# Kernel tuning notes

Measured on AMD Instinct MI355X. Metric: run time of the kernel, lower is better.

## Reference

```python
import jax, jax.numpy as jnp
import numpy as np

EMBED = 768
HEADS = 12
HEAD_DIM = EMBED // HEADS
RATES = (1, 2, 4)
SEGS = (2048, 4096, 8192)


def setup_inputs() -> dict:
    key = jax.random.key(0)
    k1, k2, k3 = jax.random.split(key, 3)
    b, n = 2, 8192
    x = jax.random.normal(k1, (b, n, EMBED), dtype=jnp.float32)
    Wqkv = jax.random.normal(k2, (3 * EMBED, EMBED), dtype=jnp.float32) * 0.02
    Wout = jax.random.normal(k3, (EMBED, EMBED), dtype=jnp.float32) * 0.02
    return {"x": x, "Wqkv": Wqkv, "Wout": Wout}


def _dilated_attention(qkv):
    # qkv: [b, n, 3, h, d]
    b, n, _, h, d = qkv.shape
    scale = 1.0 / jnp.sqrt(jnp.asarray(d, qkv.dtype))
    out = jnp.zeros((b, n, h, d), dtype=qkv.dtype)
    for r, s in zip(RATES, SEGS):
        sr = s // r
        nseg = n // s
        # strided gather: [b, nseg, sr, 3, h, d]
        g = qkv.reshape(b, nseg, s, 3, h, d)[:, :, ::r]
        # fold stride offset into batch; attention runs over the segment axis
        g = g.transpose(0, 2, 1, 3, 4, 5).reshape(b * sr, nseg, 3, h, d)
        q, k, v = g[:, :, 0], g[:, :, 1], g[:, :, 2]
        scores = jnp.einsum('bnhd,bmhd->bhnm', q, k) * scale
        attn = jax.nn.softmax(scores, axis=-1)
        o = jnp.einsum('bhnm,bmhd->bnhd', attn, v)
        # scatter-add back into strided positions
        o = o.reshape(b, sr, nseg, h, d).transpose(0, 2, 1, 3, 4)
        out = out.reshape(b, nseg, s, h, d).at[:, :, ::r].add(o).reshape(b, n, h, d)
    # normalize over full sequence dim (as in original module)
    out = out / out.sum(axis=1, keepdims=True)
    return out


def reference(x, Wqkv, Wout):
    b, n, e = x.shape
    qkv = (x @ Wqkv.T).reshape(b, n, 3, HEADS, HEAD_DIM)
    o = _dilated_attention(qkv)  # [b, n, h, d]
    return o.reshape(b, n, e) @ Wout.T
```

## Files before the change

kernel.cpp:

```cpp
#include <hip/hip_runtime.h>

typedef unsigned short u16;
typedef __attribute__((ext_vector_type(8))) short bf16x8;
typedef __attribute__((ext_vector_type(4))) float f32x4;

__device__ __forceinline__ u16 f2bf_rne(float f) {
  unsigned u = __float_as_uint(f);
  u += 0x7fffu + ((u >> 16) & 1u);
  return (u16)(u >> 16);
}
__device__ __forceinline__ float bf2f(u16 h) {
  return __uint_as_float(((unsigned)h) << 16);
}
__device__ __forceinline__ void split1(float v, u16& h, u16& l) {
  u16 hh = f2bf_rne(v);
  h = hh;
  l = f2bf_rne(v - bf2f(hh));
}

__device__ __forceinline__ void gl16(const void* g, void* l) {
  __builtin_amdgcn_global_load_lds(
      (const __attribute__((address_space(1))) unsigned int*)g,
      (__attribute__((address_space(3))) unsigned int*)l,
      16, 0, 0);
}

__global__ void split_convert_all(const float4* __restrict__ x,
                                  ushort4* __restrict__ xhi, ushort4* __restrict__ xlo,
                                  const float4* __restrict__ wq,
                                  ushort4* __restrict__ wqh, ushort4* __restrict__ wql,
                                  const float4* __restrict__ wo,
                                  ushort4* __restrict__ woh, ushort4* __restrict__ wol) {
  int i = blockIdx.x * 256 + threadIdx.x;
  const float4* src;
  ushort4 *dh, *dl;
  int idx;
  if (i < 3145728) { src = x; dh = xhi; dl = xlo; idx = i; }
  else if (i < 3588096) { src = wq; dh = wqh; dl = wql; idx = i - 3145728; }
  else if (i < 3735552) { src = wo; dh = woh; dl = wol; idx = i - 3588096; }
  else return;
  float4 v = src[idx];
  ushort4 h, l;
  split1(v.x, h.x, l.x); split1(v.y, h.y, l.y);
  split1(v.z, h.z, l.z); split1(v.w, h.w, l.w);
  dh[idx] = h; dl[idx] = l;
}

__global__ __launch_bounds__(256, 2) void gemm_split_bt(
    const u16* __restrict__ Ahi, const u16* __restrict__ Alo,
    const u16* __restrict__ Bhi, const u16* __restrict__ Blo,
    float* __restrict__ C, int M, int N, int K) {
  __shared__ __align__(16) u16 sAh[128 * 64], sAl[128 * 64], sBh[128 * 64], sBl[128 * 64];
  const int tid = threadIdx.x;
  const int wave = tid >> 6;
  const int lane = tid & 63;
  const int tm0 = blockIdx.x * 128;
  const int tn0 = blockIdx.y * 128;
  const int wm = (wave & 1) * 64;
  const int wn = (wave >> 1) * 64;

  const int srow = wave * 32 + (lane >> 3);
  const int c = lane & 7;
  const int scol = (c ^ ((lane >> 3) & 7)) * 8;
  const u16* gAh = Ahi + (size_t)(tm0 + srow) * K + scol;
  const u16* gAl = Alo + (size_t)(tm0 + srow) * K + scol;
  const u16* gBh = Bhi + (size_t)(tn0 + srow) * K + scol;
  const u16* gBl = Blo + (size_t)(tn0 + srow) * K + scol;
  u16* lAh = &sAh[wave * 32 * 64];
  u16* lAl = &sAl[wave * 32 * 64];
  u16* lBh = &sBh[wave * 32 * 64];
  u16* lBl = &sBl[wave * 32 * 64];
  const size_t rstep8 = (size_t)8 * K;

  f32x4 acc[4][4] = {};
  const int fr = lane & 15;
  const int quad = lane >> 4;

  for (int kt = 0; kt < K; kt += 64) {
#pragma unroll
    for (int r = 0; r < 4; ++r) {
      gl16(gAh + kt + r * rstep8, lAh + r * 512);
      gl16(gAl + kt + r * rstep8, lAl + r * 512);
      gl16(gBh + kt + r * rstep8, lBh + r * 512);
      gl16(gBl + kt + r * rstep8, lBl + r * 512);
    }
    __syncthreads();
    for (int subk = 0; subk < 2; ++subk) {
      const int k0 = ((subk * 4 + quad) ^ (fr & 7)) * 8;
      bf16x8 ah[4], al[4], bh[4], bl[4];
#pragma unroll
      for (int i = 0; i < 4; ++i) {
        ah[i] = *(const bf16x8*)&sAh[(wm + i * 16 + fr) * 64 + k0];
        al[i] = *(const bf16x8*)&sAl[(wm + i * 16 + fr) * 64 + k0];
        bh[i] = *(const bf16x8*)&sBh[(wn + i * 16 + fr) * 64 + k0];
        bl[i] = *(const bf16x8*)&sBl[(wn + i * 16 + fr) * 64 + k0];
      }
#pragma unroll
      for (int i = 0; i < 4; ++i)
#pragma unroll
        for (int j = 0; j < 4; ++j) {
          acc[i][j] = __builtin_amdgcn_mfma_f32_16x16x32_bf16(ah[i], bh[j], acc[i][j], 0, 0, 0);
          acc[i][j] = __builtin_amdgcn_mfma_f32_16x16x32_bf16(ah[i], bl[j], acc[i][j], 0, 0, 0);
          acc[i][j] = __builtin_amdgcn_mfma_f32_16x16x32_bf16(al[i], bh[j], acc[i][j], 0, 0, 0);
        }
    }
    __syncthreads();
  }

  const int col = lane & 15;
  const int rowq = (lane >> 4) * 4;
#pragma unroll
  for (int i = 0; i < 4; ++i)
#pragma unroll
    for (int j = 0; j < 4; ++j) {
      size_t base = (size_t)(tm0 + wm + i * 16 + rowq) * N + (tn0 + wn + j * 16 + col);
#pragma unroll
      for (int r = 0; r < 4; ++r) C[base + (size_t)r * N] = acc[i][j][r];
    }
}

__global__ __launch_bounds__(256) void attn_dilated(const float* __restrict__ qkv,
                                                    float* __restrict__ out) {
  __shared__ float rows[4][2304];
  __shared__ float sc[12][16];
  __shared__ float Aw[12][16];
  const int t = threadIdx.x;
  const int i0 = blockIdx.x;
  const int b = blockIdx.y;
  const size_t rowbase = (size_t)b * 8192 + i0;

  for (int idx = t; idx < 4 * 576; idx += 256) {
    int j = idx / 576, c4 = idx - j * 576;
    ((float4*)rows[j])[c4] = ((const float4*)(qkv + (rowbase + 2048 * j) * 2304))[c4];
  }
  __syncthreads();

  if (t < 192) {
    int h = t >> 4, j = (t >> 2) & 3, jp = t & 3;
    const float* q = &rows[j][h * 64];
    const float* k = &rows[jp][768 + h * 64];
    float s = 0.f;
#pragma unroll
    for (int d = 0; d < 64; ++d) s = fmaf(q[d], k[d], s);
    sc[h][(j << 2) | jp] = s * 0.125f;
  }
  __syncthreads();

  if (t < 48) {
    int h = t >> 2, j = t & 3;
    float s0 = sc[h][j * 4 + 0], s1 = sc[h][j * 4 + 1];
    float s2 = sc[h][j * 4 + 2], s3 = sc[h][j * 4 + 3];
    float m = fmaxf(fmaxf(s0, s1), fmaxf(s2, s3));
    float e0 = expf(s0 - m), e1 = expf(s1 - m), e2 = expf(s2 - m), e3 = expf(s3 - m);
    float inv = 1.f / (e0 + e1 + e2 + e3);
    float a[4] = {e0 * inv, e1 * inv, e2 * inv, e3 * inv};
    if ((i0 & 1) == 0) {
      int p = j ^ 2;
      float ss = sc[h][j * 4 + j], sx = sc[h][j * 4 + p];
      float mm = fmaxf(ss, sx);
      float es = expf(ss - mm), ex = expf(sx - mm);
      float iv = 1.f / (es + ex);
      a[j] += es * iv;
      a[p] += ex * iv;
    }
    if ((i0 & 3) == 0) a[j] += 1.f;
    Aw[h][j * 4 + 0] = a[0]; Aw[h][j * 4 + 1] = a[1];
    Aw[h][j * 4 + 2] = a[2]; Aw[h][j * 4 + 3] = a[3];
  }
  __syncthreads();

#pragma unroll
  for (int j = 0; j < 4; ++j) {
#pragma unroll
    for (int rep = 0; rep < 3; ++rep) {
      int cc = rep * 256 + t;
      int h = cc >> 6;
      float v = 0.f;
#pragma unroll
      for (int jp = 0; jp < 4; ++jp) v = fmaf(Aw[h][(j << 2) | jp], rows[jp][1536 + cc], v);
      out[(rowbase + 2048 * j) * 768 + cc] = v;
    }
  }
}

__global__ void colsum(const float* __restrict__ o, float* __restrict__ S) {
  int t = threadIdx.x;
  int rg = blockIdx.x;
  int cg = blockIdx.y;
  int b = blockIdx.z;
  int c = cg * 256 + t;
  const float* p = o + ((size_t)b * 8192 + (size_t)rg * 128) * 768 + c;
  float s = 0.f;
  for (int r = 0; r < 128; ++r) s += p[(size_t)r * 768];
  atomicAdd(&S[b * 768 + c], s);
}

__global__ void invk(float* S, int n) {
  int i = blockIdx.x * 256 + threadIdx.x;
  if (i < n) S[i] = 1.0f / S[i];
}

__global__ void norm_split4(const float4* __restrict__ in, const float* __restrict__ Sinv,
                            ushort4* __restrict__ hi, ushort4* __restrict__ lo, int n4) {
  int i = blockIdx.x * 256 + threadIdx.x;
  if (i >= n4) return;
  int e = i * 4;
  int c = e % 768;
  int b = e / (8192 * 768);
  const float* s = Sinv + b * 768 + c;
  float4 v = in[i];
  v.x *= s[0]; v.y *= s[1]; v.z *= s[2]; v.w *= s[3];
  ushort4 h, l;
  split1(v.x, h.x, l.x); split1(v.y, h.y, l.y);
  split1(v.z, h.z, l.z); split1(v.w, h.w, l.w);
  hi[i] = h; lo[i] = l;
}

extern "C" void kernel_launch(void* const* d_in, const int* in_sizes, int n_in,
                              void* d_out, int out_size, void* d_ws, size_t ws_size,
                              hipStream_t stream) {
  (void)in_sizes; (void)n_in; (void)out_size; (void)ws_size;
  const float* x = (const float*)d_in[0];
  const float* Wqkv = (const float*)d_in[1];
  const float* Wout = (const float*)d_in[2];
  float* out = (float*)d_out;

  char* w = (char*)d_ws;
  float* qkv = (float*)(w);
  u16* no_hi = (u16*)(w);
  u16* no_lo = (u16*)(w + 25165824);
  size_t off = 150994944;
  u16* xhi = (u16*)(w + off); off += 25165824;
  u16* xlo = (u16*)(w + off); off += 25165824;
  u16* wqh = (u16*)(w + off); off += 3538944;
  u16* wql = (u16*)(w + off); off += 3538944;
  u16* woh = (u16*)(w + off); off += 1179648;
  u16* wol = (u16*)(w + off); off += 1179648;
  float* S = (float*)(w + off); off += 6144;

  split_convert_all<<<dim3(14592), 256, 0, stream>>>(
      (const float4*)x, (ushort4*)xhi, (ushort4*)xlo,
      (const float4*)Wqkv, (ushort4*)wqh, (ushort4*)wql,
      (const float4*)Wout, (ushort4*)woh, (ushort4*)wol);

  gemm_split_bt<<<dim3(128, 18), 256, 0, stream>>>(xhi, xlo, wqh, wql, qkv, 16384, 2304, 768);

  attn_dilated<<<dim3(2048, 2), 256, 0, stream>>>(qkv, out);

  hipMemsetAsync(S, 0, 6144, stream);
  colsum<<<dim3(64, 3, 2), 256, 0, stream>>>(out, S);
  invk<<<dim3(6), 256, 0, stream>>>(S, 1536);

  norm_split4<<<dim3((3145728 + 255) / 256), 256, 0, stream>>>(
      (const float4*)out, S, (ushort4*)no_hi, (ushort4*)no_lo, 3145728);

  gemm_split_bt<<<dim3(128, 6), 256, 0, stream>>>(no_hi, no_lo, woh, wol, out, 16384, 768, 768);
}
```

Measured before the change: 381.1 us.

## Fuse column-sum into attention and switch GEMM to 32x32 MFMA tiles

Result: slower. 400.6 us (+5.1%).

```diff
diff --git a/kernel.cpp b/kernel.cpp
--- a/kernel.cpp
+++ b/kernel.cpp
@@ -2,7 +2,7 @@
 
 typedef unsigned short u16;
 typedef __attribute__((ext_vector_type(8))) short bf16x8;
-typedef __attribute__((ext_vector_type(4))) float f32x4;
+typedef __attribute__((ext_vector_type(16))) float f32x16;
 
 __device__ __forceinline__ u16 f2bf_rne(float f) {
   unsigned u = __float_as_uint(f);
@@ -72,9 +72,9 @@
   u16* lBl = &sBl[wave * 32 * 64];
   const size_t rstep8 = (size_t)8 * K;
 
-  f32x4 acc[4][4] = {};
-  const int fr = lane & 15;
-  const int quad = lane >> 4;
+  f32x16 acc[2][2] = {};
+  const int m32 = lane & 31;
+  const int half = lane >> 5;
 
   for (int kt = 0; kt < K; kt += 64) {
 #pragma unroll
@@ -85,43 +85,45 @@
       gl16(gBl + kt + r * rstep8, lBl + r * 512);
     }
     __syncthreads();
-    for (int subk = 0; subk < 2; ++subk) {
-      const int k0 = ((subk * 4 + quad) ^ (fr & 7)) * 8;
-      bf16x8 ah[4], al[4], bh[4], bl[4];
-#pragma unroll
-      for (int i = 0; i < 4; ++i) {
-        ah[i] = *(const bf16x8*)&sAh[(wm + i * 16 + fr) * 64 + k0];
-        al[i] = *(const bf16x8*)&sAl[(wm + i * 16 + fr) * 64 + k0];
-        bh[i] = *(const bf16x8*)&sBh[(wn + i * 16 + fr) * 64 + k0];
-        bl[i] = *(const bf16x8*)&sBl[(wn + i * 16 + fr) * 64 + k0];
+#pragma unroll
+    for (int ks = 0; ks < 4; ++ks) {
+      const int p = ((ks * 2 + half) ^ (lane & 7)) * 8;
+      bf16x8 ah[2], al[2], bh[2], bl[2];
+#pragma unroll
+      for (int i = 0; i < 2; ++i) {
+        ah[i] = *(const bf16x8*)&sAh[(wm + i * 32 + m32) * 64 + p];
+        al[i] = *(const bf16x8*)&sAl[(wm + i * 32 + m32) * 64 + p];
+        bh[i] = *(const bf16x8*)&sBh[(wn + i * 32 + m32) * 64 + p];
+        bl[i] = *(const bf16x8*)&sBl[(wn + i * 32 + m32) * 64 + p];
       }
 #pragma unroll
-      for (int i = 0; i < 4; ++i)
-#pragma unroll
-        for (int j = 0; j < 4; ++j) {
-          acc[i][j] = __builtin_amdgcn_mfma_f32_16x16x32_bf16(ah[i], bh[j], acc[i][j], 0, 0, 0);
-          acc[i][j] = __builtin_amdgcn_mfma_f32_16x16x32_bf16(ah[i], bl[j], acc[i][j], 0, 0, 0);
-          acc[i][j] = __builtin_amdgcn_mfma_f32_16x16x32_bf16(al[i], bh[j], acc[i][j], 0, 0, 0);
+      for (int i = 0; i < 2; ++i)
+#pragma unroll
+        for (int j = 0; j < 2; ++j) {
+          acc[i][j] = __builtin_amdgcn_mfma_f32_32x32x16_bf16(ah[i], bh[j], acc[i][j], 0, 0, 0);
+          acc[i][j] = __builtin_amdgcn_mfma_f32_32x32x16_bf16(ah[i], bl[j], acc[i][j], 0, 0, 0);
+          acc[i][j] = __builtin_amdgcn_mfma_f32_32x32x16_bf16(al[i], bh[j], acc[i][j], 0, 0, 0);
         }
     }
     __syncthreads();
   }
 
-  const int col = lane & 15;
-  const int rowq = (lane >> 4) * 4;
-#pragma unroll
-  for (int i = 0; i < 4; ++i)
-#pragma unroll
-    for (int j = 0; j < 4; ++j) {
-      size_t base = (size_t)(tm0 + wm + i * 16 + rowq) * N + (tn0 + wn + j * 16 + col);
-#pragma unroll
-      for (int r = 0; r < 4; ++r) C[base + (size_t)r * N] = acc[i][j][r];
-    }
+  const int col = lane & 31;
+#pragma unroll
+  for (int i = 0; i < 2; ++i)
+#pragma unroll
+    for (int j = 0; j < 2; ++j)
+#pragma unroll
+      for (int r = 0; r < 16; ++r) {
+        int rl = (r & 3) + 8 * (r >> 2) + 4 * half;
+        C[(size_t)(tm0 + wm + i * 32 + rl) * N + (tn0 + wn + j * 32 + col)] = acc[i][j][r];
+      }
 }
 
 __global__ __launch_bounds__(256) void attn_dilated(const float* __restrict__ qkv,
-                                                    float* __restrict__ out) {
-  __shared__ float rows[4][2304];
+                                                    float* __restrict__ out,
+                                                    float* __restrict__ Spart) {
+  __shared__ float rows[4][2312];
   __shared__ float sc[12][16];
   __shared__ float Aw[12][16];
   const int t = threadIdx.x;
@@ -137,11 +139,14 @@
 
   if (t < 192) {
     int h = t >> 4, j = (t >> 2) & 3, jp = t & 3;
-    const float* q = &rows[j][h * 64];
-    const float* k = &rows[jp][768 + h * 64];
+    const float4* q = (const float4*)&rows[j][h * 64];
+    const float4* k = (const float4*)&rows[jp][768 + h * 64];
     float s = 0.f;
 #pragma unroll
-    for (int d = 0; d < 64; ++d) s = fmaf(q[d], k[d], s);
+    for (int d = 0; d < 16; ++d) {
+      float4 a = q[d], bb = k[d];
+      s += a.x * bb.x + a.y * bb.y + a.z * bb.z + a.w * bb.w;
+    }
     sc[h][(j << 2) | jp] = s * 0.125f;
   }
   __syncthreads();
@@ -169,35 +174,33 @@
   }
   __syncthreads();
 
-#pragma unroll
-  for (int j = 0; j < 4; ++j) {
-#pragma unroll
-    for (int rep = 0; rep < 3; ++rep) {
-      int cc = rep * 256 + t;
-      int h = cc >> 6;
+  float* sp = Spart + ((size_t)b * 64 + (i0 & 63)) * 768;
+#pragma unroll
+  for (int rep = 0; rep < 3; ++rep) {
+    int cc = rep * 256 + t;
+    int h = cc >> 6;
+    float ps = 0.f;
+#pragma unroll
+    for (int j = 0; j < 4; ++j) {
       float v = 0.f;
 #pragma unroll
       for (int jp = 0; jp < 4; ++jp) v = fmaf(Aw[h][(j << 2) | jp], rows[jp][1536 + cc], v);
       out[(rowbase + 2048 * j) * 768 + cc] = v;
-    }
-  }
-}
-
-__global__ void colsum(const float* __restrict__ o, float* __restrict__ S) {
-  int t = threadIdx.x;
-  int rg = blockIdx.x;
-  int cg = blockIdx.y;
-  int b = blockIdx.z;
-  int c = cg * 256 + t;
-  const float* p = o + ((size_t)b * 8192 + (size_t)rg * 128) * 768 + c;
+      ps += v;
+    }
+    atomicAdd(&sp[cc], ps);
+  }
+}
+
+__global__ void colred(const float* __restrict__ Spart, float* __restrict__ Sinv) {
+  int i = blockIdx.x * 256 + threadIdx.x;
+  if (i >= 1536) return;
+  int b = i / 768, c = i - b * 768;
+  const float* p = Spart + (size_t)b * 64 * 768 + c;
   float s = 0.f;
-  for (int r = 0; r < 128; ++r) s += p[(size_t)r * 768];
-  atomicAdd(&S[b * 768 + c], s);
-}
-
-__global__ void invk(float* S, int n) {
-  int i = blockIdx.x * 256 + threadIdx.x;
-  if (i < n) S[i] = 1.0f / S[i];
+#pragma unroll
+  for (int g = 0; g < 64; ++g) s += p[g * 768];
+  Sinv[i] = 1.0f / s;
 }
 
 __global__ void norm_split4(const float4* __restrict__ in, const float* __restrict__ Sinv,
@@ -230,13 +233,15 @@
   u16* no_hi = (u16*)(w);
   u16* no_lo = (u16*)(w + 25165824);
   size_t off = 150994944;
-  u16* xhi = (u16*)(w + off); off += 25165824;
+  u16* xhi = (u16*)(w + off);
+  float* Spart = (float*)(w + off);
+  float* Sinv = (float*)(w + off + 393216);
+  off += 25165824;
   u16* xlo = (u16*)(w + off); off += 25165824;
   u16* wqh = (u16*)(w + off); off += 3538944;
   u16* wql = (u16*)(w + off); off += 3538944;
   u16* woh = (u16*)(w + off); off += 1179648;
   u16* wol = (u16*)(w + off); off += 1179648;
-  float* S = (float*)(w + off); off += 6144;
 
   split_convert_all<<<dim3(14592), 256, 0, stream>>>(
       (const float4*)x, (ushort4*)xhi, (ushort4*)xlo,
@@ -245,14 +250,13 @@
 
   gemm_split_bt<<<dim3(128, 18), 256, 0, stream>>>(xhi, xlo, wqh, wql, qkv, 16384, 2304, 768);
 
-  attn_dilated<<<dim3(2048, 2), 256, 0, stream>>>(qkv, out);
-
-  hipMemsetAsync(S, 0, 6144, stream);
-  colsum<<<dim3(64, 3, 2), 256, 0, stream>>>(out, S);
-  invk<<<dim3(6), 256, 0, stream>>>(S, 1536);
+  hipMemsetAsync(Spart, 0, 393216, stream);
+  attn_dilated<<<dim3(2048, 2), 256, 0, stream>>>(qkv, out, Spart);
+
+  colred<<<dim3(6), 256, 0, stream>>>(Spart, Sinv);
 
   norm_split4<<<dim3((3145728 + 255) / 256), 256, 0, stream>>>(
-      (const float4*)out, S, (ushort4*)no_hi, (ushort4*)no_lo, 3145728);
+      (const float4*)out, Sinv, (ushort4*)no_hi, (ushort4*)no_lo, 3145728);
 
   gemm_split_bt<<<dim3(128, 6), 256, 0, stream>>>(no_hi, no_lo, woh, wol, out, 16384, 768, 768);
 }
```

## Fold column normalization into Wout and fuse attention output with bf16 split

Applied to the files above, without the earlier changes.

Measured after the change: 351.4 us. 1.08x faster.

```diff
diff --git a/kernel.cpp b/kernel.cpp
--- a/kernel.cpp
+++ b/kernel.cpp
@@ -28,16 +28,13 @@
 __global__ void split_convert_all(const float4* __restrict__ x,
                                   ushort4* __restrict__ xhi, ushort4* __restrict__ xlo,
                                   const float4* __restrict__ wq,
-                                  ushort4* __restrict__ wqh, ushort4* __restrict__ wql,
-                                  const float4* __restrict__ wo,
-                                  ushort4* __restrict__ woh, ushort4* __restrict__ wol) {
+                                  ushort4* __restrict__ wqh, ushort4* __restrict__ wql) {
   int i = blockIdx.x * 256 + threadIdx.x;
   const float4* src;
   ushort4 *dh, *dl;
   int idx;
   if (i < 3145728) { src = x; dh = xhi; dl = xlo; idx = i; }
   else if (i < 3588096) { src = wq; dh = wqh; dl = wql; idx = i - 3145728; }
-  else if (i < 3735552) { src = wo; dh = woh; dl = wol; idx = i - 3588096; }
   else return;
   float4 v = src[idx];
   ushort4 h, l;
@@ -47,8 +44,9 @@
 }
 
 __global__ __launch_bounds__(256, 2) void gemm_split_bt(
-    const u16* __restrict__ Ahi, const u16* __restrict__ Alo,
+    const u16* __restrict__ Ahi, const u16* __restrict__ Alo, int lda,
     const u16* __restrict__ Bhi, const u16* __restrict__ Blo,
+    const u16* __restrict__ Bhi2, const u16* __restrict__ Blo2,
     float* __restrict__ C, int M, int N, int K) {
   __shared__ __align__(16) u16 sAh[128 * 64], sAl[128 * 64], sBh[128 * 64], sBl[128 * 64];
   const int tid = threadIdx.x;
@@ -58,19 +56,21 @@
   const int tn0 = blockIdx.y * 128;
   const int wm = (wave & 1) * 64;
   const int wn = (wave >> 1) * 64;
+  if (2 * tm0 >= M) { Bhi = Bhi2; Blo = Blo2; }
 
   const int srow = wave * 32 + (lane >> 3);
   const int c = lane & 7;
   const int scol = (c ^ ((lane >> 3) & 7)) * 8;
-  const u16* gAh = Ahi + (size_t)(tm0 + srow) * K + scol;
-  const u16* gAl = Alo + (size_t)(tm0 + srow) * K + scol;
+  const u16* gAh = Ahi + (size_t)(tm0 + srow) * lda + scol;
+  const u16* gAl = Alo + (size_t)(tm0 + srow) * lda + scol;
   const u16* gBh = Bhi + (size_t)(tn0 + srow) * K + scol;
   const u16* gBl = Blo + (size_t)(tn0 + srow) * K + scol;
   u16* lAh = &sAh[wave * 32 * 64];
   u16* lAl = &sAl[wave * 32 * 64];
   u16* lBh = &sBh[wave * 32 * 64];
   u16* lBl = &sBl[wave * 32 * 64];
-  const size_t rstep8 = (size_t)8 * K;
+  const size_t rstepA = (size_t)8 * lda;
+  const size_t rstepB = (size_t)8 * K;
 
   f32x4 acc[4][4] = {};
   const int fr = lane & 15;
@@ -79,10 +79,10 @@
   for (int kt = 0; kt < K; kt += 64) {
 #pragma unroll
     for (int r = 0; r < 4; ++r) {
-      gl16(gAh + kt + r * rstep8, lAh + r * 512);
-      gl16(gAl + kt + r * rstep8, lAl + r * 512);
-      gl16(gBh + kt + r * rstep8, lBh + r * 512);
-      gl16(gBl + kt + r * rstep8, lBl + r * 512);
+      gl16(gAh + kt + r * rstepA, lAh + r * 512);
+      gl16(gAl + kt + r * rstepA, lAl + r * 512);
+      gl16(gBh + kt + r * rstepB, lBh + r * 512);
+      gl16(gBl + kt + r * rstepB, lBl + r * 512);
     }
     __syncthreads();
     for (int subk = 0; subk < 2; ++subk) {
@@ -120,8 +120,9 @@
 }
 
 __global__ __launch_bounds__(256) void attn_dilated(const float* __restrict__ qkv,
-                                                    float* __restrict__ out) {
-  __shared__ float rows[4][2304];
+                                                    u16* __restrict__ qk16,
+                                                    float* __restrict__ Spart) {
+  __shared__ float rows[4][2312];
   __shared__ float sc[12][16];
   __shared__ float Aw[12][16];
   const int t = threadIdx.x;
@@ -137,11 +138,14 @@
 
   if (t < 192) {
     int h = t >> 4, j = (t >> 2) & 3, jp = t & 3;
-    const float* q = &rows[j][h * 64];
-    const float* k = &rows[jp][768 + h * 64];
+    const float4* q = (const float4*)&rows[j][h * 64];
+    const float4* k = (const float4*)&rows[jp][768 + h * 64];
     float s = 0.f;
 #pragma unroll
-    for (int d = 0; d < 64; ++d) s = fmaf(q[d], k[d], s);
+    for (int d = 0; d < 16; ++d) {
+      float4 a = q[d], bb = k[d];
+      s += a.x * bb.x + a.y * bb.y + a.z * bb.z + a.w * bb.w;
+    }
     sc[h][(j << 2) | jp] = s * 0.125f;
   }
   __syncthreads();
@@ -169,51 +173,55 @@
   }
   __syncthreads();
 
-#pragma unroll
-  for (int j = 0; j < 4; ++j) {
-#pragma unroll
-    for (int rep = 0; rep < 3; ++rep) {
-      int cc = rep * 256 + t;
-      int h = cc >> 6;
+  float* sp = Spart + ((size_t)b * 64 + (i0 & 63)) * 768;
+#pragma unroll
+  for (int rep = 0; rep < 3; ++rep) {
+    int cc = rep * 256 + t;
+    int h = cc >> 6;
+    float ps = 0.f;
+#pragma unroll
+    for (int j = 0; j < 4; ++j) {
       float v = 0.f;
 #pragma unroll
       for (int jp = 0; jp < 4; ++jp) v = fmaf(Aw[h][(j << 2) | jp], rows[jp][1536 + cc], v);
-      out[(rowbase + 2048 * j) * 768 + cc] = v;
-    }
-  }
-}
-
-__global__ void colsum(const float* __restrict__ o, float* __restrict__ S) {
-  int t = threadIdx.x;
-  int rg = blockIdx.x;
-  int cg = blockIdx.y;
-  int b = blockIdx.z;
-  int c = cg * 256 + t;
-  const float* p = o + ((size_t)b * 8192 + (size_t)rg * 128) * 768 + c;
+      u16 h16, l16;
+      split1(v, h16, l16);
+      size_t base = (rowbase + 2048 * j) * 4608;
+      qk16[base + cc] = h16;
+      qk16[base + 768 + cc] = l16;
+      ps += v;
+    }
+    atomicAdd(&sp[cc], ps);
+  }
+}
+
+__global__ void colred(const float* __restrict__ Spart, float* __restrict__ Sinv) {
+  int i = blockIdx.x * 256 + threadIdx.x;
+  if (i >= 1536) return;
+  int b = i / 768, c = i - b * 768;
+  const float* p = Spart + (size_t)b * 64 * 768 + c;
   float s = 0.f;
-  for (int r = 0; r < 128; ++r) s += p[(size_t)r * 768];
-  atomicAdd(&S[b * 768 + c], s);
-}
-
-__global__ void invk(float* S, int n) {
+#pragma unroll
+  for (int g = 0; g < 64; ++g) s += p[g * 768];
+  Sinv[i] = 1.0f / s;
+}
+
+__global__ void scale_wout(const float4* __restrict__ Wout, const float* __restrict__ Sinv,
+                           ushort4* __restrict__ wh0, ushort4* __restrict__ wl0,
+                           ushort4* __restrict__ wh1, ushort4* __restrict__ wl1) {
   int i = blockIdx.x * 256 + threadIdx.x;
-  if (i < n) S[i] = 1.0f / S[i];
-}
-
-__global__ void norm_split4(const float4* __restrict__ in, const float* __restrict__ Sinv,
-                            ushort4* __restrict__ hi, ushort4* __restrict__ lo, int n4) {
-  int i = blockIdx.x * 256 + threadIdx.x;
-  if (i >= n4) return;
-  int e = i * 4;
-  int c = e % 768;
-  int b = e / (8192 * 768);
+  if (i >= 294912) return;
+  int b = i / 147456;
+  int r = i - b * 147456;
+  int c = (r % 192) * 4;
   const float* s = Sinv + b * 768 + c;
-  float4 v = in[i];
+  float4 v = Wout[r];
   v.x *= s[0]; v.y *= s[1]; v.z *= s[2]; v.w *= s[3];
   ushort4 h, l;
   split1(v.x, h.x, l.x); split1(v.y, h.y, l.y);
   split1(v.z, h.z, l.z); split1(v.w, h.w, l.w);
-  hi[i] = h; lo[i] = l;
+  if (b == 0) { wh0[r] = h; wl0[r] = l; }
+  else        { wh1[r] = h; wl1[r] = l; }
 }
 
 extern "C" void kernel_launch(void* const* d_in, const int* in_sizes, int n_in,
@@ -227,32 +235,37 @@
 
   char* w = (char*)d_ws;
   float* qkv = (float*)(w);
-  u16* no_hi = (u16*)(w);
-  u16* no_lo = (u16*)(w + 25165824);
+  u16* qk16 = (u16*)(w);
   size_t off = 150994944;
-  u16* xhi = (u16*)(w + off); off += 25165824;
+  u16* xhi = (u16*)(w + off);
+  float* Spart = (float*)(w + off);
+  float* Sinv = (float*)(w + off + 393216);
+  u16* wh0 = (u16*)(w + off + 400000);
+  u16* wl0 = (u16*)(w + off + 1579648);
+  u16* wh1 = (u16*)(w + off + 2759296);
+  u16* wl1 = (u16*)(w + off + 3938944);
+  off += 25165824;
   u16* xlo = (u16*)(w + off); off += 25165824;
   u16* wqh = (u16*)(w + off); off += 3538944;
   u16* wql = (u16*)(w + off); off += 3538944;
-  u16* woh = (u16*)(w + off); off += 1179648;
-  u16* wol = (u16*)(w + off); off += 1179648;
-  float* S = (float*)(w + off); off += 6144;
-
-  split_convert_all<<<dim3(14592), 256, 0, stream>>>(
+
+  split_convert_all<<<dim3(14016), 256, 0, stream>>>(
       (const float4*)x, (ushort4*)xhi, (ushort4*)xlo,
-      (const float4*)Wqkv, (ushort4*)wqh, (ushort4*)wql,
-      (const float4*)Wout, (ushort4*)woh, (ushort4*)wol);
-
-  gemm_split_bt<<<dim3(128, 18), 256, 0, stream>>>(xhi, xlo, wqh, wql, qkv, 16384, 2304, 768);
-
-  attn_dilated<<<dim3(2048, 2), 256, 0, stream>>>(qkv, out);
-
-  hipMemsetAsync(S, 0, 6144, stream);
-  colsum<<<dim3(64, 3, 2), 256, 0, stream>>>(out, S);
-  invk<<<dim3(6), 256, 0, stream>>>(S, 1536);
-
-  norm_split4<<<dim3((3145728 + 255) / 256), 256, 0, stream>>>(
-      (const float4*)out, S, (ushort4*)no_hi, (ushort4*)no_lo, 3145728);
-
-  gemm_split_bt<<<dim3(128, 6), 256, 0, stream>>>(no_hi, no_lo, woh, wol, out, 16384, 768, 768);
-}
+      (const float4*)Wqkv, (ushort4*)wqh, (ushort4*)wql);
+
+  gemm_split_bt<<<dim3(128, 18), 256, 0, stream>>>(xhi, xlo, 768, wqh, wql, wqh, wql,
+                                                   qkv, 16384, 2304, 768);
+
+  hipMemsetAsync(Spart, 0, 393216, stream);
+  attn_dilated<<<dim3(2048, 2), 256, 0, stream>>>(qkv, qk16, Spart);
+
+  colred<<<dim3(6), 256, 0, stream>>>(Spart, Sinv);
+
+  scale_wout<<<dim3(1152), 256, 0, stream>>>((const float4*)Wout, Sinv,
+                                             (ushort4*)wh0, (ushort4*)wl0,
+                                             (ushort4*)wh1, (ushort4*)wl1);
+
+  gemm_split_bt<<<dim3(128, 6), 256, 0, stream>>>(qk16, qk16 + 768, 4608,
+                                                  wh0, wl0, wh1, wl1,
+                                                  out, 16384, 768, 768);
+}
```
